# Optimization experiments

Measured on AMD Instinct MI355X. Metric: run time of the kernel, lower is better.

The kernel has to match this reference:

```python
import jax, jax.numpy as jnp
import numpy as np

N = 100000      # nodes
E = 1600000     # edges (before self-loops)
FIN = 128       # in_channels
HID = 16        # hidden_channels
H = 8           # heads (layer 1)
OUT = 64        # out_channels
LN_EPS = 1e-5


def setup_inputs() -> dict:
    key = jax.random.key(0)
    ks = jax.random.split(key, 24)
    def p(i, shape):
        return jax.random.normal(ks[i], shape, dtype=jnp.float32) * 0.05
    return {
        "x": jax.random.normal(ks[0], (N, FIN), dtype=jnp.float32),
        "edge_index": jax.random.randint(ks[1], (2, E), 0, N, dtype=jnp.int32),
        # GATv2 layer 1: in -> H*HID, concat
        "Wl1": p(2, (FIN, H * HID)), "bl1": p(3, (H * HID,)),
        "Wr1": p(4, (FIN, H * HID)), "br1": p(5, (H * HID,)),
        "att1": p(6, (H, HID)), "bias1": p(7, (H * HID,)),
        # GATv2 layer 2: H*HID -> HID, heads=1
        "Wl2": p(8, (H * HID, HID)), "bl2": p(9, (HID,)),
        "Wr2": p(10, (H * HID, HID)), "br2": p(11, (HID,)),
        "att2": p(12, (1, HID)), "bias2": p(13, (HID,)),
        # LayerNorms
        "ln1_g": jnp.ones((H * HID,), jnp.float32), "ln1_b": jnp.zeros((H * HID,), jnp.float32),
        "ln2_g": jnp.ones((HID,), jnp.float32), "ln2_b": jnp.zeros((HID,), jnp.float32),
        # residual / skip / output linears
        "res1_W": p(14, (FIN, H * HID)), "res1_b": p(15, (H * HID,)),
        "res2_W": p(16, (H * HID, HID)), "res2_b": p(17, (HID,)),
        "skip_W": p(18, (H * HID, HID)), "skip_b": p(19, (HID,)),
        "out_W": p(20, (HID, OUT)), "out_b": p(21, (OUT,)),
    }


def _layernorm(x, g, b):
    mu = jnp.mean(x, axis=-1, keepdims=True)
    var = jnp.mean((x - mu) ** 2, axis=-1, keepdims=True)
    return (x - mu) * jax.lax.rsqrt(var + LN_EPS) * g + b


def _gatv2(x, src, dst, Wl, bl, Wr, br, att, bias, concat):
    # PyG GATv2Conv (share_weights=False, eval mode): message from src j to dst i
    Hh, C = att.shape
    n = x.shape[0]
    xl = (x @ Wl + bl).reshape(n, Hh, C)   # source-side transform
    xr = (x @ Wr + br).reshape(n, Hh, C)   # target-side transform
    m = xl[src] + xr[dst]                  # [E, H, C]
    e = jax.nn.leaky_relu(m, 0.2)
    alpha = jnp.einsum('ehc,hc->eh', e, att)          # [E, H]
    amax = jax.ops.segment_max(alpha, dst, num_segments=n)
    alpha = jnp.exp(alpha - amax[dst])
    denom = jax.ops.segment_sum(alpha, dst, num_segments=n)
    alpha = alpha / (denom[dst] + 1e-16)
    out = jax.ops.segment_sum(xl[src] * alpha[:, :, None], dst, num_segments=n)  # [N, H, C]
    out = out.reshape(n, Hh * C) if concat else out.mean(axis=1)
    return out + bias


def reference(x, edge_index, Wl1, bl1, Wr1, br1, att1, bias1,
              Wl2, bl2, Wr2, br2, att2, bias2,
              ln1_g, ln1_b, ln2_g, ln2_b,
              res1_W, res1_b, res2_W, res2_b, skip_W, skip_b, out_W, out_b):
    n = x.shape[0]
    loops = jnp.arange(n, dtype=edge_index.dtype)
    src = jnp.concatenate([edge_index[0], loops])
    dst = jnp.concatenate([edge_index[1], loops])

    h = _gatv2(x, src, dst, Wl1, bl1, Wr1, br1, att1, bias1, concat=True)
    h = _layernorm(h, ln1_g, ln1_b)
    h = h + (x @ res1_W + res1_b)
    h = jax.nn.elu(h)            # dropout off in eval

    skip_in = h
    h2 = _gatv2(h, src, dst, Wl2, bl2, Wr2, br2, att2, bias2, concat=False)
    h2 = _layernorm(h2, ln2_g, ln2_b)
    h2 = h2 + (skip_in @ res2_W + res2_b)
    h2 = jax.nn.elu(h2)
    h2 = h2 + (skip_in @ skip_W + skip_b)
    return h2 @ out_W + out_b
```

## Files before the change

kernel.cpp:

```cpp
#include <hip/hip_runtime.h>

typedef __attribute__((ext_vector_type(8))) short bf16x8;
typedef __attribute__((ext_vector_type(4))) float f32x4;

__device__ __forceinline__ float bf2f(ushort u) {
  union { uint i; float f; } v; v.i = ((uint)u) << 16; return v.f;
}
__device__ __forceinline__ ushort f2bf(float f) {
  union { float f; uint i; } v; v.f = f;
  uint r = (v.i + 0x7FFFu + ((v.i >> 16) & 1u)) >> 16;
  return (ushort)r;
}
__device__ __forceinline__ float blo(uint u) { return __builtin_bit_cast(float, u << 16); }
__device__ __forceinline__ float bhi(uint u) { return __builtin_bit_cast(float, u & 0xffff0000u); }

template <int CTRL>
__device__ __forceinline__ float dppadd(float x) {
  union { float f; int i; } a, b;
  a.f = x;
  b.i = __builtin_amdgcn_update_dpp(0, a.i, CTRL, 0xF, 0xF, true);
  return a.f + b.f;
}
#define DPP_X1 0xB1
#define DPP_X2 0x4E
#define DPP_X7 0x141
#define DPP_XF 0x140


__global__ __launch_bounds__(256) void k_init(
    const float* __restrict__ Wl1, const float* __restrict__ bl1,
    const float* __restrict__ Wr1, const float* __restrict__ br1,
    const float* __restrict__ res1W, const float* __restrict__ res1b,
    const float* __restrict__ Wl2, const float* __restrict__ bl2,
    const float* __restrict__ Wr2, const float* __restrict__ br2,
    const float* __restrict__ res2W, const float* __restrict__ res2b,
    const float* __restrict__ skipW, const float* __restrict__ skipb,
    const float* __restrict__ att1, const float* __restrict__ att2,
    ushort* __restrict__ W1F, float* __restrict__ B1P,
    ushort* __restrict__ W2F, float* __restrict__ B2P,
    float* __restrict__ at6, float* __restrict__ at4, float* __restrict__ at2E,
    int* __restrict__ cnt, int N) {
  const float LOG2E = 1.4426950408889634f;
  int b = blockIdx.x, t = threadIdx.x;
  if (b < 227) {
    int tid = b * 256 + t;
    if (tid < 49152) {
      int j = tid & 7, l = (tid >> 3) & 63, ktile = (tid >> 9) & 3, ct = tid >> 11;
      int k = ktile * 32 + ((l >> 4) << 3) + j;
      int n = ct * 16 + (l & 15);
      int sel = n >> 7, jj = n & 127;
      const float* s = sel == 0 ? Wl1 : sel == 1 ? Wr1 : res1W;
      W1F[tid] = f2bf(s[k * 128 + jj]);
    } else if (tid < 57344) {
      int u = tid - 49152;
      int j = u & 7, l = (u >> 3) & 63, ktile = (u >> 9) & 3, ct = u >> 11;
      int k = ktile * 32 + ((l >> 4) << 3) + j;
      int n = ct * 16 + (l & 15);
      int sel = n >> 4, jj = n & 15;
      const float* s = sel == 0 ? Wl2 : sel == 1 ? Wr2 : sel == 2 ? res2W : skipW;
      W2F[u] = f2bf(s[k * 16 + jj]);
    } else if (tid < 57728) {
      int n = tid - 57344;
      int sel = n >> 7, jj = n & 127;
      const float* sb = sel == 0 ? bl1 : sel == 1 ? br1 : res1b;
      B1P[n] = sb[jj];
    } else if (tid < 57792) {
      int n = tid - 57728;
      int sel = n >> 4, jj = n & 15;
      const float* sb = sel == 0 ? bl2 : sel == 1 ? br2 : sel == 2 ? res2b : skipb;
      B2P[n] = sb[jj];
    } else if (tid < 57920) {
      int n = tid - 57792;
      at6[n] = att1[n] * 0.6f * LOG2E;
    } else if (tid < 58048) {
      int n = tid - 57920;
      at4[n] = att1[n] * 0.4f * LOG2E;
    } else if (tid < 58064) {
      int n = tid - 58048;
      at2E[n] = att2[n] * LOG2E;
    }
  } else {
    int idx = (b - 227) * 256 + t;
    if (idx < N) cnt[idx] = 0;
  }
}


__global__ __launch_bounds__(256) void k_histgemm(
    const int* __restrict__ ei, int* __restrict__ cnt, int E, int nh,
    const float* __restrict__ x, const ushort* __restrict__ WF,
    const float* __restrict__ bias,
    ushort* __restrict__ O0, ushort* __restrict__ O1, ushort* __restrict__ O2,
    int M) {
  __shared__ ushort LT[64 * 136];
  int b = blockIdx.x, t = threadIdx.x;
  if (b < nh) {
    int e4 = (b * 256 + t) * 4;
    if (e4 + 3 < E) {
      int4 d = *(const int4*)&ei[E + e4];
      atomicAdd(&cnt[d.x], 1); atomicAdd(&cnt[d.y], 1);
      atomicAdd(&cnt[d.z], 1); atomicAdd(&cnt[d.w], 1);
    } else {
      for (int e = e4; e < E; ++e) atomicAdd(&cnt[ei[E + e]], 1);
    }
    return;
  }
  int w = t >> 6, l = t & 63;
  int m0 = (b - nh) * 64;
  int rql = l & 15, kq = l >> 4;
  bf16x8 afr[16];
  #pragma unroll
  for (int kt = 0; kt < 4; ++kt) {
    #pragma unroll
    for (int rt = 0; rt < 4; ++rt) {
      int m = m0 + rt * 16 + rql;
      uint4 o = make_uint4(0, 0, 0, 0);
      if (m < M) {
        const float* src = x + (size_t)m * 128 + kt * 32 + kq * 8;
        float4 f0 = *(const float4*)src;
        float4 f1 = *(const float4*)(src + 4);
        o.x = f2bf(f0.x) | ((uint)f2bf(f0.y) << 16);
        o.y = f2bf(f0.z) | ((uint)f2bf(f0.w) << 16);
        o.z = f2bf(f1.x) | ((uint)f2bf(f1.y) << 16);
        o.w = f2bf(f1.z) | ((uint)f2bf(f1.w) << 16);
      }
      afr[kt * 4 + rt] = __builtin_bit_cast(bf16x8, o);
    }
  }
  #pragma unroll
  for (int a = 0; a < 3; ++a) {
    #pragma unroll
    for (int c2 = 0; c2 < 2; ++c2) {
      int ctl = w * 2 + c2;
      int ct = a * 8 + ctl;
      int col = ctl * 16 + rql;
      float bv = bias[a * 128 + col];
      f32x4 acc[4] = {};
      #pragma unroll
      for (int kt = 0; kt < 4; ++kt) {
        bf16x8 bfrag = *(const bf16x8*)(WF + ((size_t)((ct * 4 + kt) * 64 + l)) * 8);
        #pragma unroll
        for (int rt = 0; rt < 4; ++rt)
          acc[rt] = __builtin_amdgcn_mfma_f32_16x16x32_bf16(afr[kt * 4 + rt], bfrag, acc[rt], 0, 0, 0);
      }
      #pragma unroll
      for (int rt = 0; rt < 4; ++rt)
        #pragma unroll
        for (int r = 0; r < 4; ++r)
          LT[(rt * 16 + kq * 4 + r) * 136 + col] = f2bf(acc[rt][r] + bv);
    }
    __syncthreads();
    ushort* O = a == 0 ? O0 : a == 1 ? O1 : O2;
    #pragma unroll
    for (int it = 0; it < 4; ++it) {
      int idx = it * 256 + t;
      int row = idx >> 4, seg = idx & 15;
      int m = m0 + row;
      if (m < M) {
        uint4 v = *(const uint4*)&LT[row * 136 + seg * 8];
        *(uint4*)&O[(size_t)m * 128 + seg * 8] = v;
      }
    }
    __syncthreads();
  }
}


__global__ __launch_bounds__(256) void k_scan1(const int* __restrict__ cnt, int* __restrict__ partial, int n) {
  int i = blockIdx.x * 256 + threadIdx.x;
  int v = (i < n) ? cnt[i] : 0;
  #pragma unroll
  for (int m = 1; m < 64; m <<= 1) v += __shfl_xor(v, m);
  __shared__ int sm[4];
  if ((threadIdx.x & 63) == 0) sm[threadIdx.x >> 6] = v;
  __syncthreads();
  if (threadIdx.x == 0) partial[blockIdx.x] = sm[0] + sm[1] + sm[2] + sm[3];
}


__global__ __launch_bounds__(256) void k_scan3lb(const int* __restrict__ cnt, const int* __restrict__ partial,
                                                 int* __restrict__ rowptr, int* __restrict__ cursor, int n) {
  int t = threadIdx.x;
  int b = blockIdx.x;
  int acc = 0;
  for (int j = t; j < b; j += 256) acc += partial[j];
  #pragma unroll
  for (int m = 1; m < 64; m <<= 1) acc += __shfl_xor(acc, m);
  __shared__ int sm[4];
  if ((t & 63) == 0) sm[t >> 6] = acc;
  __syncthreads();
  int base = sm[0] + sm[1] + sm[2] + sm[3];
  __shared__ int buf[2][256];
  int i = b * 256 + t;
  int v = (i < n) ? cnt[i] : 0;
  buf[0][t] = v;
  __syncthreads();
  int cur = 0;
  for (int off = 1; off < 256; off <<= 1) {
    int x = buf[cur][t];
    if (t >= off) x += buf[cur][t - off];
    buf[cur ^ 1][t] = x;
    __syncthreads();
    cur ^= 1;
  }
  if (i < n) {
    int incl = buf[cur][t];
    int rp = base + incl - v;
    rowptr[i] = rp;
    cursor[i] = rp;
    if (i == n - 1) rowptr[n] = base + incl;
  }
}


__global__ __launch_bounds__(256) void k_scatter(const int* __restrict__ ei, int* __restrict__ cursor,
                                                 int* __restrict__ ssrc, int E, int NS) {
  int t = threadIdx.x;
  int base = blockIdx.x * 2048;
  int src[8], dst[8];
  #pragma unroll
  for (int j = 0; j < 8; ++j) {
    int idx = base + j * 256 + t;
    bool ok = idx < E;
    src[j] = ok ? ei[idx] : 0;
    dst[j] = ok ? ei[E + idx] : -1;
  }
  for (int s = 0; s < NS; ++s) {
    #pragma unroll
    for (int j = 0; j < 8; ++j) {
      if ((dst[j] >> 13) == s) {
        int pos = atomicAdd(&cursor[dst[j]], 1);
        ssrc[pos] = src[j];
      }
    }
  }
}


__global__ __launch_bounds__(256) void k_mfma2(
    const ushort* __restrict__ AF, const ushort* __restrict__ WF,
    const float* __restrict__ bias,
    ushort* __restrict__ O0, ushort* __restrict__ O1,
    ushort* __restrict__ O2, ushort* __restrict__ O3, int M) {
  int w = threadIdx.x >> 6, l = threadIdx.x & 63;
  int m0 = blockIdx.x * 64;
  int c0 = w * 16;
  int ct = c0 >> 4;
  f32x4 acc[4] = {};
  #pragma unroll
  for (int kt = 0; kt < 4; ++kt) {
    bf16x8 b = *(const bf16x8*)(WF + ((size_t)((ct * 4 + kt) * 64 + l)) * 8);
    #pragma unroll
    for (int rt = 0; rt < 4; ++rt) {
      bf16x8 a = *(const bf16x8*)(AF + ((size_t)((blockIdx.x * 16 + rt * 4 + kt) * 64 + l)) * 8);
      acc[rt] = __builtin_amdgcn_mfma_f32_16x16x32_bf16(a, b, acc[rt], 0, 0, 0);
    }
  }
  int col = c0 + (l & 15);
  int arr = col >> 4;
  ushort* O = arr == 0 ? O0 : arr == 1 ? O1 : arr == 2 ? O2 : O3;
  int lcol = col & 15;
  float bv = bias[col];
  int rbase = m0 + ((l >> 4) << 2);
  #pragma unroll
  for (int rt = 0; rt < 4; ++rt) {
    #pragma unroll
    for (int r = 0; r < 4; ++r) {
      int m = rbase + rt * 16 + r;
      if (m < M) O[(size_t)m * 16 + lcol] = f2bf(acc[rt][r] + bv);
    }
  }
}


#define EDGE1B(u, MASKHI)                                              \
  {                                                                    \
    float v0 = blo((u).x), v1 = bhi((u).x);                            \
    float v2 = blo((u).y), v3 = bhi((u).y);                            \
    float m0 = v0 + xr0, m1 = v1 + xr1, m2 = v2 + xr2, m3 = v3 + xr3;  \
    float d = a6.x * m0 + a4.x * __builtin_fabsf(m0);                  \
    d += a6.y * m1; d += a4.y * __builtin_fabsf(m1);                   \
    d += a6.z * m2; d += a4.z * __builtin_fabsf(m2);                   \
    d += a6.w * m3; d += a4.w * __builtin_fabsf(m3);                   \
    d = dppadd<DPP_X1>(d);                                             \
    d = dppadd<DPP_X2>(d);                                             \
    float p = __builtin_amdgcn_exp2f(d);                               \
    if (MASKHI) p = hi ? 0.f : p;                                      \
    acc0 += p * v0; acc1 += p * v1; acc2 += p * v2; acc3 += p * v3;    \
    den += p;                                                          \
  }

__global__ __launch_bounds__(256) void k_gat1(
    const ushort* __restrict__ XLG, const ushort* __restrict__ XR,
    const ushort* __restrict__ RE,
    const float* __restrict__ at6, const float* __restrict__ at4,
    const float* __restrict__ bias1,
    const float* __restrict__ g1, const float* __restrict__ b1,
    const int* __restrict__ rowptr, const int* __restrict__ ssrc,
    ushort* __restrict__ HF, int n) {
  int lane = threadIdx.x & 63;
  int i = blockIdx.x * 4 + (threadIdx.x >> 6);
  if (i >= n) return;
  int l32 = lane & 31;
  bool hi = lane >= 32;
  int hioff4 = (lane & 32) >> 3;
  int fbb = l32 << 3;
  int fb = l32 * 4;
  size_t rowb = (size_t)i << 8;
  uint2 uxr = *(const uint2*)((const char*)XR + rowb + fbb);
  float xr0 = blo(uxr.x), xr1 = bhi(uxr.x), xr2 = blo(uxr.y), xr3 = bhi(uxr.y);
  float4 a6 = *(const float4*)&at6[fb];
  float4 a4 = *(const float4*)&at4[fb];
  float acc0 = 0.f, acc1 = 0.f, acc2 = 0.f, acc3 = 0.f, den = 0.f;
  {
    uint2 us = *(const uint2*)((const char*)XLG + rowb + fbb);
    EDGE1B(us, true);
  }
  int e0 = __builtin_amdgcn_readfirstlane(rowptr[i]);
  int e1 = __builtin_amdgcn_readfirstlane(rowptr[i + 1]);
  for (int base = e0; base < e1; base += 64) {
    int cnt = e1 - base; if (cnt > 64) cnt = 64;
    int sidx = ssrc[base + (lane < cnt ? lane : cnt - 1)];
    int j = 0;
    for (; j + 16 <= cnt; j += 16) {
      uint o0 = (uint)__builtin_amdgcn_ds_bpermute(((j + 0)  << 2) + hioff4, sidx) << 8;
      uint o1 = (uint)__builtin_amdgcn_ds_bpermute(((j + 2)  << 2) + hioff4, sidx) << 8;
      uint o2 = (uint)__builtin_amdgcn_ds_bpermute(((j + 4)  << 2) + hioff4, sidx) << 8;
      uint o3 = (uint)__builtin_amdgcn_ds_bpermute(((j + 6)  << 2) + hioff4, sidx) << 8;
      uint o4 = (uint)__builtin_amdgcn_ds_bpermute(((j + 8)  << 2) + hioff4, sidx) << 8;
      uint o5 = (uint)__builtin_amdgcn_ds_bpermute(((j + 10) << 2) + hioff4, sidx) << 8;
      uint o6 = (uint)__builtin_amdgcn_ds_bpermute(((j + 12) << 2) + hioff4, sidx) << 8;
      uint o7 = (uint)__builtin_amdgcn_ds_bpermute(((j + 14) << 2) + hioff4, sidx) << 8;
      uint2 u0 = *(const uint2*)((const char*)XLG + o0 + fbb);
      uint2 u1 = *(const uint2*)((const char*)XLG + o1 + fbb);
      uint2 u2 = *(const uint2*)((const char*)XLG + o2 + fbb);
      uint2 u3 = *(const uint2*)((const char*)XLG + o3 + fbb);
      uint2 u4 = *(const uint2*)((const char*)XLG + o4 + fbb);
      uint2 u5 = *(const uint2*)((const char*)XLG + o5 + fbb);
      uint2 u6 = *(const uint2*)((const char*)XLG + o6 + fbb);
      uint2 u7 = *(const uint2*)((const char*)XLG + o7 + fbb);
      EDGE1B(u0, false); EDGE1B(u1, false); EDGE1B(u2, false); EDGE1B(u3, false);
      EDGE1B(u4, false); EDGE1B(u5, false); EDGE1B(u6, false); EDGE1B(u7, false);
    }
    for (; j + 8 <= cnt; j += 8) {
      uint o0 = (uint)__builtin_amdgcn_ds_bpermute(((j + 0) << 2) + hioff4, sidx) << 8;
      uint o1 = (uint)__builtin_amdgcn_ds_bpermute(((j + 2) << 2) + hioff4, sidx) << 8;
      uint o2 = (uint)__builtin_amdgcn_ds_bpermute(((j + 4) << 2) + hioff4, sidx) << 8;
      uint o3 = (uint)__builtin_amdgcn_ds_bpermute(((j + 6) << 2) + hioff4, sidx) << 8;
      uint2 u0 = *(const uint2*)((const char*)XLG + o0 + fbb);
      uint2 u1 = *(const uint2*)((const char*)XLG + o1 + fbb);
      uint2 u2 = *(const uint2*)((const char*)XLG + o2 + fbb);
      uint2 u3 = *(const uint2*)((const char*)XLG + o3 + fbb);
      EDGE1B(u0, false); EDGE1B(u1, false); EDGE1B(u2, false); EDGE1B(u3, false);
    }
    for (; j + 2 <= cnt; j += 2) {
      uint o = (uint)__builtin_amdgcn_ds_bpermute((j << 2) + hioff4, sidx) << 8;
      uint2 u = *(const uint2*)((const char*)XLG + o + fbb);
      EDGE1B(u, false);
    }
    if (j < cnt) {
      uint o = (uint)__builtin_amdgcn_ds_bpermute((j << 2) + hioff4, sidx) << 8;
      uint2 u = *(const uint2*)((const char*)XLG + o + fbb);
      EDGE1B(u, true);
    }
  }
  acc0 += __shfl_xor(acc0, 32);
  acc1 += __shfl_xor(acc1, 32);
  acc2 += __shfl_xor(acc2, 32);
  acc3 += __shfl_xor(acc3, 32);
  den  += __shfl_xor(den, 32);
  float inv = 1.f / (den + 1e-16f);
  float4 bv = *(const float4*)&bias1[fb];
  float o0 = acc0 * inv + bv.x, o1 = acc1 * inv + bv.y;
  float o2 = acc2 * inv + bv.z, o3 = acc3 * inv + bv.w;
  float s = o0 + o1 + o2 + o3;
  #pragma unroll
  for (int m = 1; m < 32; m <<= 1) s += __shfl_xor(s, m);
  float mu = s * (1.f / 128.f);
  float d0 = o0 - mu, d1 = o1 - mu, d2 = o2 - mu, d3 = o3 - mu;
  float q = d0 * d0 + d1 * d1 + d2 * d2 + d3 * d3;
  #pragma unroll
  for (int m = 1; m < 32; m <<= 1) q += __shfl_xor(q, m);
  float rstd = rsqrtf(q * (1.f / 128.f) + 1e-5f);
  float4 gg = *(const float4*)&g1[fb];
  float4 bb = *(const float4*)&b1[fb];
  uint2 ur = *(const uint2*)((const char*)RE + rowb + fbb);
  float r0 = blo(ur.x), r1 = bhi(ur.x), r2 = blo(ur.y), r3 = bhi(ur.y);
  float y0 = d0 * rstd * gg.x + bb.x + r0;
  float y1 = d1 * rstd * gg.y + bb.y + r1;
  float y2 = d2 * rstd * gg.z + bb.z + r2;
  float y3 = d3 * rstd * gg.w + bb.w + r3;
  y0 = y0 > 0.f ? y0 : __expf(y0) - 1.f;
  y1 = y1 > 0.f ? y1 : __expf(y1) - 1.f;
  y2 = y2 > 0.f ? y2 : __expf(y2) - 1.f;
  y3 = y3 > 0.f ? y3 : __expf(y3) - 1.f;
  if (!hi) {
    int k8 = l32 >> 1;
    size_t slot = ((size_t)(i >> 4) * 4 + (k8 >> 2)) * 64 + (i & 15) + ((k8 & 3) << 4);
    uint2 o;
    o.x = (uint)f2bf(y0) | ((uint)f2bf(y1) << 16);
    o.y = (uint)f2bf(y2) | ((uint)f2bf(y3) << 16);
    *(uint2*)(HF + slot * 8 + (l32 & 1) * 4) = o;
  }
}


#define EDGE2V(v)                                            \
  {                                                          \
    float m = (v) + xr;                                      \
    float ta = a2 * m;                                       \
    float tb = a2 * __builtin_fabsf(m);                      \
    float tt = 0.6f * ta + 0.4f * tb;                        \
    tt = dppadd<DPP_X1>(tt);                                 \
    tt = dppadd<DPP_X2>(tt);                                 \
    tt = dppadd<DPP_X7>(tt);                                 \
    tt = dppadd<DPP_XF>(tt);                                 \
    float p = __builtin_amdgcn_exp2f(tt);                    \
    acc += p * (v); den += p;                                \
  }

__global__ __launch_bounds__(256) void k_gat2(
    const ushort* __restrict__ XG, const ushort* __restrict__ XRr,
    const ushort* __restrict__ XE, const ushort* __restrict__ XS,
    const float* __restrict__ at2E, const float* __restrict__ bias2,
    const float* __restrict__ g2, const float* __restrict__ b2,
    const int* __restrict__ rowptr, const int* __restrict__ ssrc,
    const float* __restrict__ outW, const float* __restrict__ outB,
    float* __restrict__ Out, int n) {
  __shared__ float sW[1024];
  __shared__ float sB[64];
  int t = threadIdx.x;
  for (int idx = t; idx < 1024; idx += 256) sW[idx] = outW[idx];
  if (t < 64) sB[t] = outB[t];
  __syncthreads();
  int c = t & 15;
  int i = blockIdx.x * 16 + (t >> 4);
  if (i >= n) return;
  size_t ib = (size_t)i << 4;
  float xl = bf2f(XG[ib + c]), xr = bf2f(XRr[ib + c]);
  float resv = bf2f(XE[ib + c]), skipv = bf2f(XS[ib + c]);
  float a2 = at2E[c];
  float acc = 0.f, den = 0.f;
  EDGE2V(xl);
  int e0 = rowptr[i], e1 = rowptr[i + 1];
  int e = e0;
  for (; e + 8 <= e1; e += 8) {
    int s0 = ssrc[e],     s1 = ssrc[e + 1], s2 = ssrc[e + 2], s3 = ssrc[e + 3];
    int s4 = ssrc[e + 4], s5 = ssrc[e + 5], s6 = ssrc[e + 6], s7 = ssrc[e + 7];
    float v0 = bf2f(XG[((size_t)(uint)s0 << 4) + c]);
    float v1 = bf2f(XG[((size_t)(uint)s1 << 4) + c]);
    float v2 = bf2f(XG[((size_t)(uint)s2 << 4) + c]);
    float v3 = bf2f(XG[((size_t)(uint)s3 << 4) + c]);
    float v4 = bf2f(XG[((size_t)(uint)s4 << 4) + c]);
    float v5 = bf2f(XG[((size_t)(uint)s5 << 4) + c]);
    float v6 = bf2f(XG[((size_t)(uint)s6 << 4) + c]);
    float v7 = bf2f(XG[((size_t)(uint)s7 << 4) + c]);
    EDGE2V(v0); EDGE2V(v1); EDGE2V(v2); EDGE2V(v3);
    EDGE2V(v4); EDGE2V(v5); EDGE2V(v6); EDGE2V(v7);
  }
  for (; e < e1; ++e) {
    int s = ssrc[e];
    float v = bf2f(XG[((size_t)(uint)s << 4) + c]);
    EDGE2V(v);
  }
  float o = acc / (den + 1e-16f) + bias2[c];
  float s = o;
  s = dppadd<DPP_X1>(s); s = dppadd<DPP_X2>(s); s = dppadd<DPP_X7>(s); s = dppadd<DPP_XF>(s);
  float mu = s * (1.f / 16.f);
  float d = o - mu;
  float q = d * d;
  q = dppadd<DPP_X1>(q); q = dppadd<DPP_X2>(q); q = dppadd<DPP_X7>(q); q = dppadd<DPP_XF>(q);
  float rstd = rsqrtf(q * (1.f / 16.f) + 1e-5f);
  float y = d * rstd * g2[c] + b2[c] + resv;
  y = y > 0.f ? y : __expf(y) - 1.f;
  y += skipv;
  float a0 = sB[c * 4 + 0], a1 = sB[c * 4 + 1], ao2 = sB[c * 4 + 2], a3 = sB[c * 4 + 3];
  #pragma unroll
  for (int cc = 0; cc < 16; ++cc) {
    float h = __shfl(y, cc, 16);
    a0 += h * sW[cc * 64 + c * 4 + 0];
    a1 += h * sW[cc * 64 + c * 4 + 1];
    ao2 += h * sW[cc * 64 + c * 4 + 2];
    a3 += h * sW[cc * 64 + c * 4 + 3];
  }
  *(float4*)&Out[(size_t)i * 64 + c * 4] = make_float4(a0, a1, ao2, a3);
}


extern "C" void kernel_launch(void* const* d_in, const int* in_sizes, int n_in,
                              void* d_out, int out_size, void* d_ws, size_t ws_size,
                              hipStream_t stream) {
  const float* x     = (const float*)d_in[0];
  const int*   ei    = (const int*)d_in[1];
  const float* Wl1   = (const float*)d_in[2];
  const float* bl1   = (const float*)d_in[3];
  const float* Wr1   = (const float*)d_in[4];
  const float* br1   = (const float*)d_in[5];
  const float* att1  = (const float*)d_in[6];
  const float* bias1 = (const float*)d_in[7];
  const float* Wl2   = (const float*)d_in[8];
  const float* bl2   = (const float*)d_in[9];
  const float* Wr2   = (const float*)d_in[10];
  const float* br2   = (const float*)d_in[11];
  const float* att2  = (const float*)d_in[12];
  const float* bias2 = (const float*)d_in[13];
  const float* ln1g  = (const float*)d_in[14];
  const float* ln1b  = (const float*)d_in[15];
  const float* ln2g  = (const float*)d_in[16];
  const float* ln2b  = (const float*)d_in[17];
  const float* res1W = (const float*)d_in[18];
  const float* res1b = (const float*)d_in[19];
  const float* res2W = (const float*)d_in[20];
  const float* res2b = (const float*)d_in[21];
  const float* skipW = (const float*)d_in[22];
  const float* skipb = (const float*)d_in[23];
  const float* outW  = (const float*)d_in[24];
  const float* outb  = (const float*)d_in[25];
  int N = in_sizes[0] / 128;
  int E = in_sizes[1] / 2;
  float* out = (float*)d_out;

  int nblk = (N + 63) / 64;
  int ngrp = nblk * 4;

  ushort* XLG  = (ushort*)d_ws;
  ushort* XR1  = XLG + (size_t)N * 128;
  ushort* RE1  = XR1 + (size_t)N * 128;
  ushort* HF   = RE1 + (size_t)N * 128;
  ushort* XG2  = HF + (size_t)ngrp * 2048;
  ushort* X2R  = XG2 + (size_t)N * 16;
  ushort* X2E  = X2R + (size_t)N * 16;
  ushort* X2S  = X2E + (size_t)N * 16;
  ushort* W1F  = X2S + (size_t)N * 16;
  ushort* W2F  = W1F + 49152;
  float*  B1P  = (float*)(W2F + 8192);
  float*  B2P  = B1P + 384;
  float*  at6  = B2P + 64;
  float*  at4  = at6 + 128;
  float*  at2E = at4 + 128;
  int* cnt     = (int*)(at2E + 16);
  int* cursor  = cnt + N;
  int* rowptr  = cursor + N;
  int* ssrc    = rowptr + N + 1;
  int* partial = ssrc + E;

  int nbS = (N + 255) / 256;
  int NS  = ((N - 1) >> 13) + 1;
  int nScat = (E + 2047) / 2048;
  int nh = (E + 1023) / 1024;

  k_init<<<227 + nbS, 256, 0, stream>>>(Wl1, bl1, Wr1, br1, res1W, res1b,
                                        Wl2, bl2, Wr2, br2, res2W, res2b, skipW, skipb,
                                        att1, att2, W1F, B1P, W2F, B2P, at6, at4, at2E,
                                        cnt, N);
  k_histgemm<<<nh + nblk, 256, 0, stream>>>(ei, cnt, E, nh, x, W1F, B1P,
                                            XLG, XR1, RE1, N);
  k_scan1<<<nbS, 256, 0, stream>>>(cnt, partial, N);
  k_scan3lb<<<nbS, 256, 0, stream>>>(cnt, partial, rowptr, cursor, N);
  k_scatter<<<nScat, 256, 0, stream>>>(ei, cursor, ssrc, E, NS);
  k_gat1<<<(N + 3) / 4, 256, 0, stream>>>(XLG, XR1, RE1, at6, at4, bias1, ln1g, ln1b,
                                          rowptr, ssrc, HF, N);
  k_mfma2<<<nblk, 256, 0, stream>>>(HF, W2F, B2P, XG2, X2R, X2E, X2S, N);
  k_gat2<<<(N + 15) / 16, 256, 0, stream>>>(XG2, X2R, X2E, X2S, at2E, bias2, ln2g, ln2b,
                                            rowptr, ssrc, outW, outb, out, N);
}
```

Baseline: 477.6 us.

## Split histogram from GEMM, privatize counters, pre-convert x to bf16 fragments

The fused histogram+GEMM kernel is split. A new kernel pairs the degree histogram with conversion of x into bf16 MFMA-fragment layout, and the histogram now uses 8 privatized count arrays to reduce atomic contention. The scan sums the 8 copies. The layer-1 GEMM becomes a separate kernel that loads the pre-laid-out fragments, placed after the scatter. This adds an extra write and read of x in bf16, plus a larger zeroing pass, in exchange for less atomic contention and simpler GEMM loads.

```diff
diff --git a/kernel.cpp b/kernel.cpp
--- a/kernel.cpp
+++ b/kernel.cpp
@@ -39,7 +39,7 @@
     ushort* __restrict__ W1F, float* __restrict__ B1P,
     ushort* __restrict__ W2F, float* __restrict__ B2P,
     float* __restrict__ at6, float* __restrict__ at4, float* __restrict__ at2E,
-    int* __restrict__ cnt, int N) {
+    int* __restrict__ cnt8, int N) {
   const float LOG2E = 1.4426950408889634f;
   int b = blockIdx.x, t = threadIdx.x;
   if (b < 227) {
@@ -81,20 +81,17 @@
     }
   } else {
     int idx = (b - 227) * 256 + t;
-    if (idx < N) cnt[idx] = 0;
-  }
-}
-
-
-__global__ __launch_bounds__(256) void k_histgemm(
-    const int* __restrict__ ei, int* __restrict__ cnt, int E, int nh,
-    const float* __restrict__ x, const ushort* __restrict__ WF,
-    const float* __restrict__ bias,
-    ushort* __restrict__ O0, ushort* __restrict__ O1, ushort* __restrict__ O2,
-    int M) {
-  __shared__ ushort LT[64 * 136];
+    if (idx < 8 * N) cnt8[idx] = 0;
+  }
+}
+
+
+__global__ __launch_bounds__(256) void k_convhist(
+    const int* __restrict__ ei, int* __restrict__ cnt8, int E, int nh, int N,
+    const float* __restrict__ x, ushort* __restrict__ XF) {
   int b = blockIdx.x, t = threadIdx.x;
   if (b < nh) {
+    int* cnt = cnt8 + (size_t)(b & 7) * N;
     int e4 = (b * 256 + t) * 4;
     if (e4 + 3 < E) {
       int4 d = *(const int4*)&ei[E + e4];
@@ -105,28 +102,114 @@
     }
     return;
   }
-  int w = t >> 6, l = t & 63;
-  int m0 = (b - nh) * 64;
+  int t2 = (b - nh) * 256 + t;
+  if (t2 >= N * 16) return;
+  int m = t2 >> 4, k8 = t2 & 15;
+  const float* src = x + (size_t)m * 128 + k8 * 8;
+  float4 f0 = *(const float4*)src;
+  float4 f1 = *(const float4*)(src + 4);
+  uint4 o;
+  o.x = f2bf(f0.x) | ((uint)f2bf(f0.y) << 16);
+  o.y = f2bf(f0.z) | ((uint)f2bf(f0.w) << 16);
+  o.z = f2bf(f1.x) | ((uint)f2bf(f1.y) << 16);
+  o.w = f2bf(f1.z) | ((uint)f2bf(f1.w) << 16);
+  size_t off = ((size_t)(((m >> 4) * 4 + (k8 >> 2)) * 64) + (m & 15) + ((k8 & 3) << 4)) * 8;
+  *(uint4*)(XF + off) = o;
+}
+
+
+__global__ __launch_bounds__(256) void k_scan1(const int* __restrict__ cnt8, int* __restrict__ cntS,
+                                               int* __restrict__ partial, int n) {
+  int i = blockIdx.x * 256 + threadIdx.x;
+  int v = 0;
+  if (i < n) {
+    #pragma unroll
+    for (int c = 0; c < 8; ++c) v += cnt8[(size_t)c * n + i];
+    cntS[i] = v;
+  }
+  #pragma unroll
+  for (int m = 1; m < 64; m <<= 1) v += __shfl_xor(v, m);
+  __shared__ int sm[4];
+  if ((threadIdx.x & 63) == 0) sm[threadIdx.x >> 6] = v;
+  __syncthreads();
+  if (threadIdx.x == 0) partial[blockIdx.x] = sm[0] + sm[1] + sm[2] + sm[3];
+}
+
+
+__global__ __launch_bounds__(256) void k_scan3lb(const int* __restrict__ cntS, const int* __restrict__ partial,
+                                                 int* __restrict__ rowptr, int* __restrict__ cursor, int n) {
+  int t = threadIdx.x;
+  int b = blockIdx.x;
+  int acc = 0;
+  for (int j = t; j < b; j += 256) acc += partial[j];
+  #pragma unroll
+  for (int m = 1; m < 64; m <<= 1) acc += __shfl_xor(acc, m);
+  __shared__ int sm[4];
+  if ((t & 63) == 0) sm[t >> 6] = acc;
+  __syncthreads();
+  int base = sm[0] + sm[1] + sm[2] + sm[3];
+  __shared__ int buf[2][256];
+  int i = b * 256 + t;
+  int v = (i < n) ? cntS[i] : 0;
+  buf[0][t] = v;
+  __syncthreads();
+  int cur = 0;
+  for (int off = 1; off < 256; off <<= 1) {
+    int x = buf[cur][t];
+    if (t >= off) x += buf[cur][t - off];
+    buf[cur ^ 1][t] = x;
+    __syncthreads();
+    cur ^= 1;
+  }
+  if (i < n) {
+    int incl = buf[cur][t];
+    int rp = base + incl - v;
+    rowptr[i] = rp;
+    cursor[i] = rp;
+    if (i == n - 1) rowptr[n] = base + incl;
+  }
+}
+
+
+__global__ __launch_bounds__(256) void k_scatter(const int* __restrict__ ei, int* __restrict__ cursor,
+                                                 int* __restrict__ ssrc, int E, int NS) {
+  int t = threadIdx.x;
+  int base = blockIdx.x * 2048;
+  int src[8], dst[8];
+  #pragma unroll
+  for (int j = 0; j < 8; ++j) {
+    int idx = base + j * 256 + t;
+    bool ok = idx < E;
+    src[j] = ok ? ei[idx] : 0;
+    dst[j] = ok ? ei[E + idx] : -1;
+  }
+  for (int s = 0; s < NS; ++s) {
+    #pragma unroll
+    for (int j = 0; j < 8; ++j) {
+      if ((dst[j] >> 13) == s) {
+        int pos = atomicAdd(&cursor[dst[j]], 1);
+        ssrc[pos] = src[j];
+      }
+    }
+  }
+}
+
+
+__global__ __launch_bounds__(256) void k_gemm1(
+    const ushort* __restrict__ XF, const ushort* __restrict__ WF,
+    const float* __restrict__ bias,
+    ushort* __restrict__ O0, ushort* __restrict__ O1, ushort* __restrict__ O2,
+    int M) {
+  __shared__ ushort LT[64 * 136];
+  int t = threadIdx.x, w = t >> 6, l = t & 63;
+  int m0 = blockIdx.x * 64;
   int rql = l & 15, kq = l >> 4;
   bf16x8 afr[16];
   #pragma unroll
-  for (int kt = 0; kt < 4; ++kt) {
-    #pragma unroll
-    for (int rt = 0; rt < 4; ++rt) {
-      int m = m0 + rt * 16 + rql;
-      uint4 o = make_uint4(0, 0, 0, 0);
-      if (m < M) {
-        const float* src = x + (size_t)m * 128 + kt * 32 + kq * 8;
-        float4 f0 = *(const float4*)src;
-        float4 f1 = *(const float4*)(src + 4);
-        o.x = f2bf(f0.x) | ((uint)f2bf(f0.y) << 16);
-        o.y = f2bf(f0.z) | ((uint)f2bf(f0.w) << 16);
-        o.z = f2bf(f1.x) | ((uint)f2bf(f1.y) << 16);
-        o.w = f2bf(f1.z) | ((uint)f2bf(f1.w) << 16);
-      }
-      afr[kt * 4 + rt] = __builtin_bit_cast(bf16x8, o);
-    }
-  }
+  for (int kt = 0; kt < 4; ++kt)
+    #pragma unroll
+    for (int rt = 0; rt < 4; ++rt)
+      afr[kt * 4 + rt] = *(const bf16x8*)(XF + ((size_t)((blockIdx.x * 16 + rt * 4 + kt) * 64 + l)) * 8);
   #pragma unroll
   for (int a = 0; a < 3; ++a) {
     #pragma unroll
@@ -162,77 +245,6 @@
       }
     }
     __syncthreads();
-  }
-}
-
-
-__global__ __launch_bounds__(256) void k_scan1(const int* __restrict__ cnt, int* __restrict__ partial, int n) {
-  int i = blockIdx.x * 256 + threadIdx.x;
-  int v = (i < n) ? cnt[i] : 0;
-  #pragma unroll
-  for (int m = 1; m < 64; m <<= 1) v += __shfl_xor(v, m);
-  __shared__ int sm[4];
-  if ((threadIdx.x & 63) == 0) sm[threadIdx.x >> 6] = v;
-  __syncthreads();
-  if (threadIdx.x == 0) partial[blockIdx.x] = sm[0] + sm[1] + sm[2] + sm[3];
-}
-
-
-__global__ __launch_bounds__(256) void k_scan3lb(const int* __restrict__ cnt, const int* __restrict__ partial,
-                                                 int* __restrict__ rowptr, int* __restrict__ cursor, int n) {
-  int t = threadIdx.x;
-  int b = blockIdx.x;
-  int acc = 0;
-  for (int j = t; j < b; j += 256) acc += partial[j];
-  #pragma unroll
-  for (int m = 1; m < 64; m <<= 1) acc += __shfl_xor(acc, m);
-  __shared__ int sm[4];
-  if ((t & 63) == 0) sm[t >> 6] = acc;
-  __syncthreads();
-  int base = sm[0] + sm[1] + sm[2] + sm[3];
-  __shared__ int buf[2][256];
-  int i = b * 256 + t;
-  int v = (i < n) ? cnt[i] : 0;
-  buf[0][t] = v;
-  __syncthreads();
-  int cur = 0;
-  for (int off = 1; off < 256; off <<= 1) {
-    int x = buf[cur][t];
-    if (t >= off) x += buf[cur][t - off];
-    buf[cur ^ 1][t] = x;
-    __syncthreads();
-    cur ^= 1;
-  }
-  if (i < n) {
-    int incl = buf[cur][t];
-    int rp = base + incl - v;
-    rowptr[i] = rp;
-    cursor[i] = rp;
-    if (i == n - 1) rowptr[n] = base + incl;
-  }
-}
-
-
-__global__ __launch_bounds__(256) void k_scatter(const int* __restrict__ ei, int* __restrict__ cursor,
-                                                 int* __restrict__ ssrc, int E, int NS) {
-  int t = threadIdx.x;
-  int base = blockIdx.x * 2048;
-  int src[8], dst[8];
-  #pragma unroll
-  for (int j = 0; j < 8; ++j) {
-    int idx = base + j * 256 + t;
-    bool ok = idx < E;
-    src[j] = ok ? ei[idx] : 0;
-    dst[j] = ok ? ei[E + idx] : -1;
-  }
-  for (int s = 0; s < NS; ++s) {
-    #pragma unroll
-    for (int j = 0; j < 8; ++j) {
-      if ((dst[j] >> 13) == s) {
-        int pos = atomicAdd(&cursor[dst[j]], 1);
-        ssrc[pos] = src[j];
-      }
-    }
   }
 }
 
@@ -523,7 +535,8 @@
   int nblk = (N + 63) / 64;
   int ngrp = nblk * 4;
 
-  ushort* XLG  = (ushort*)d_ws;
+  ushort* XF   = (ushort*)d_ws;
+  ushort* XLG  = XF + (size_t)ngrp * 2048;
   ushort* XR1  = XLG + (size_t)N * 128;
   ushort* RE1  = XR1 + (size_t)N * 128;
   ushort* HF   = RE1 + (size_t)N * 128;
@@ -538,8 +551,9 @@
   float*  at6  = B2P + 64;
   float*  at4  = at6 + 128;
   float*  at2E = at4 + 128;
-  int* cnt     = (int*)(at2E + 16);
-  int* cursor  = cnt + N;
+  int* cnt8    = (int*)(at2E + 16);
+  int* cntS    = cnt8 + (size_t)8 * N;
+  int* cursor  = cntS + N;
   int* rowptr  = cursor + N;
   int* ssrc    = rowptr + N + 1;
   int* partial = ssrc + E;
@@ -547,17 +561,19 @@
   int nbS = (N + 255) / 256;
   int NS  = ((N - 1) >> 13) + 1;
   int nScat = (E + 2047) / 2048;
-  int nh = (E + 1023) / 1024;
-
-  k_init<<<227 + nbS, 256, 0, stream>>>(Wl1, bl1, Wr1, br1, res1W, res1b,
+  int nh  = (E + 1023) / 1024;
+  int CB  = (N * 16 + 255) / 256;
+  int nbZ = (8 * N + 255) / 256;
+
+  k_init<<<227 + nbZ, 256, 0, stream>>>(Wl1, bl1, Wr1, br1, res1W, res1b,
                                         Wl2, bl2, Wr2, br2, res2W, res2b, skipW, skipb,
                                         att1, att2, W1F, B1P, W2F, B2P, at6, at4, at2E,
-                                        cnt, N);
-  k_histgemm<<<nh + nblk, 256, 0, stream>>>(ei, cnt, E, nh, x, W1F, B1P,
-                                            XLG, XR1, RE1, N);
-  k_scan1<<<nbS, 256, 0, stream>>>(cnt, partial, N);
-  k_scan3lb<<<nbS, 256, 0, stream>>>(cnt, partial, rowptr, cursor, N);
+                                        cnt8, N);
+  k_convhist<<<nh + CB, 256, 0, stream>>>(ei, cnt8, E, nh, N, x, XF);
+  k_scan1<<<nbS, 256, 0, stream>>>(cnt8, cntS, partial, N);
+  k_scan3lb<<<nbS, 256, 0, stream>>>(cntS, partial, rowptr, cursor, N);
   k_scatter<<<nScat, 256, 0, stream>>>(ei, cursor, ssrc, E, NS);
+  k_gemm1<<<nblk, 256, 0, stream>>>(XF, W1F, B1P, XLG, XR1, RE1, N);
   k_gat1<<<(N + 3) / 4, 256, 0, stream>>>(XLG, XR1, RE1, at6, at4, bias1, ln1g, ln1b,
                                           rowptr, ssrc, HF, N);
   k_mfma2<<<nblk, 256, 0, stream>>>(HF, W2F, B2P, XG2, X2R, X2E, X2S, N);
```

Measured after the change: 469.3 us. Within noise of the previous version (-1.7%).
